# Performance work log

Measured on AMD Instinct MI355X. Metric: run time of the kernel, lower is better.

Reference implementation:

```python
import jax, jax.numpy as jnp
import numpy as np


def _slice_coeffs(grid, guide):
    """Trilinear slice of bilateral grid at (x, y, guide) per full-res pixel.
    grid:  [B, C, D, Hg, Wg]  (C=12 affine coeffs)
    guide: [B, 1, H, W] in [0, 1]
    returns coeffs [B, C, H, W]
    """
    B, C, D, Hg, Wg = grid.shape
    H, W = guide.shape[2], guide.shape[3]
    g = guide[:, 0]  # [B, H, W]

    # HDRNet sampling convention: pixel centers mapped into grid coords
    gx = (jnp.arange(W, dtype=grid.dtype) + 0.5) / W * Wg - 0.5   # [W]
    gy = (jnp.arange(H, dtype=grid.dtype) + 0.5) / H * Hg - 0.5   # [H]
    gz = g * D - 0.5                                              # [B, H, W]

    gx = jnp.broadcast_to(gx[None, None, :], (B, H, W))
    gy = jnp.broadcast_to(gy[None, :, None], (B, H, W))

    fx0 = jnp.floor(gx); fy0 = jnp.floor(gy); fz0 = jnp.floor(gz)
    wx = gx - fx0; wy = gy - fy0; wz = gz - fz0  # trilinear fractions

    x0 = jnp.clip(fx0.astype(jnp.int32), 0, Wg - 1)
    x1 = jnp.clip(fx0.astype(jnp.int32) + 1, 0, Wg - 1)
    y0 = jnp.clip(fy0.astype(jnp.int32), 0, Hg - 1)
    y1 = jnp.clip(fy0.astype(jnp.int32) + 1, 0, Hg - 1)
    z0 = jnp.clip(fz0.astype(jnp.int32), 0, D - 1)
    z1 = jnp.clip(fz0.astype(jnp.int32) + 1, 0, D - 1)

    def gather_one(gb, zi, yi, xi):
        # gb: [C, D, Hg, Wg]; zi/yi/xi: [H, W] -> [C, H, W]
        return gb[:, zi, yi, xi]

    gather = jax.vmap(gather_one)  # over batch

    out = jnp.zeros((B, C, H, W), dtype=grid.dtype)
    for zi, wzc in ((z0, 1.0 - wz), (z1, wz)):
        for yi, wyc in ((y0, 1.0 - wy), (y1, wy)):
            for xi, wxc in ((x0, 1.0 - wx), (x1, wx)):
                w = (wzc * wyc * wxc)[:, None]  # [B, 1, H, W]
                out = out + w * gather(grid, zi, yi, xi)
    return out


def setup_inputs() -> dict:
    key = jax.random.key(0)
    k1, k2, k3 = jax.random.split(key, 3)
    Bilterial_Grid = jax.random.normal(k1, (4, 12, 8, 16, 16), dtype=jnp.float32)
    Guide = jax.random.uniform(k2, (4, 1, 1024, 1024), dtype=jnp.float32)
    fr = jax.random.uniform(k3, (4, 3, 1024, 1024), dtype=jnp.float32)
    return {"Bilterial_Grid": Bilterial_Grid, "Guide": Guide, "fr": fr}


def reference(Bilterial_Grid, Guide, fr):
    B, _, H, W = fr.shape
    coeffs = _slice_coeffs(Bilterial_Grid, Guide)          # [B, 12, H, W]
    co = coeffs.reshape(B, 3, 4, H, W)                      # 3x4 affine per pixel
    # out_c = sum_i A[c,i] * fr_i + b[c]
    out = jnp.einsum('boihw,bihw->bohw', co[:, :, :3], fr) + co[:, :, 3]
    return out
```

## Files before the change

### kernel.cpp

```cpp
#include <hip/hip_runtime.h>


#define ZSTRIDE 132

static __device__ __forceinline__ unsigned short f2bf(float f) {
    unsigned int u = __float_as_uint(f);
    u += ((u >> 16) & 1u) + 0x7FFFu;
    return (unsigned short)(u >> 16);
}
static __device__ __forceinline__ float bf_lo(unsigned int d) {
    return __uint_as_float(d << 16);
}
static __device__ __forceinline__ float bf_hi(unsigned int d) {
    return __uint_as_float(d & 0xFFFF0000u);
}

static __device__ __forceinline__ void corner_fma(
    const unsigned int* __restrict__ cp, float wl, float wh,
    float& a0, float& a1, float& a2, float& a3)
{
    const uint4 d = *reinterpret_cast<const uint4*>(cp);
    a0 = fmaf(wl, bf_lo(d.x), a0); a0 = fmaf(wh, bf_hi(d.x), a0);
    a1 = fmaf(wl, bf_lo(d.y), a1); a1 = fmaf(wh, bf_hi(d.y), a1);
    a2 = fmaf(wl, bf_lo(d.z), a2); a2 = fmaf(wh, bf_hi(d.z), a2);
    a3 = fmaf(wl, bf_lo(d.w), a3); a3 = fmaf(wh, bf_hi(d.w), a3);
}

__global__ __launch_bounds__(256, 3) void slice_apply(
    const float* __restrict__ grid,
    const float* __restrict__ guide,
    const float* __restrict__ fr,
    float* __restrict__ out)
{
    __shared__ __align__(16) unsigned int lds[8 * ZSTRIDE];

    const int b     = blockIdx.y;
    const int tileX = blockIdx.x & 15;
    const int tileY = blockIdx.x >> 4;
    const int t     = threadIdx.x;

    {
        const int py0 = min(max(tileY - 1, 0), 15);
        const int py1 = tileY;
        const int py2 = min(tileY + 1, 15);
        const int px0 = min(max(tileX - 1, 0), 15);
        const int px1 = tileX;
        const int px2 = min(tileX + 1, 15);
        for (int e = t; e < 8 * 9 * 12; e += 256) {
            const int c    = e % 12;
            const int cell = (e / 12) % 9;
            const int s    = e / 108;
            const int s2   = min(s + 1, 7);
            const int gy3  = cell / 3;
            const int gx3  = cell % 3;
            const int ry = (gy3 == 0) ? py0 : ((gy3 == 1) ? py1 : py2);
            const int rx = (gx3 == 0) ? px0 : ((gx3 == 1) ? px1 : px2);
            const int cb = (b * 12 + c) * 8;
            const int sp = ry * 16 + rx;
            const float lo = grid[(cb + s)  * 256 + sp];
            const float hi = grid[(cb + s2) * 256 + sp];
            lds[s * ZSTRIDE + cell * 12 + c] =
                (unsigned int)f2bf(lo) | ((unsigned int)f2bf(hi) << 16);
        }
    }
    __syncthreads();

    const int w   = t >> 6;
    const int l   = t & 63;
    const int by  = w >> 1;
    const int bx  = w & 1;
    const int lxq = l & 31;
    const int sub = l >> 5;

    const int xg = tileX * 64 + bx * 32 + lxq;
    const float wx = ((float)(bx * 32 + lxq) + 0.5f) * 0.015625f +
                     (0.5f - (float)bx);
    const float u1 = wx, u0 = 1.0f - wx;

    const int cof0 = ((by + 0) * 3 + (bx + 0)) * 12;
    const int cof1 = ((by + 0) * 3 + (bx + 1)) * 12;
    const int cof2 = ((by + 1) * 3 + (bx + 0)) * 12;
    const int cof3 = ((by + 1) * 3 + (bx + 1)) * 12;

    const int ybase = tileY * 64 + by * 32;

    for (int i = 0; i < 16; ++i) {
        const int ly = by * 32 + i * 2 + sub;
        const int y  = ybase - by * 32 + ly;
        const float wy = ((float)ly + 0.5f) * 0.015625f + (0.5f - (float)by);
        const float v1 = wy, v0 = 1.0f - wy;

        const int gofs = (b * 1024 + y) * 1024 + xg;
        const int fofs = ((b * 3) * 1024 + y) * 1024 + xg;

        const float g  = guide[gofs];
        const float f0 = fr[fofs];
        const float f1 = fr[fofs + 1048576];
        const float f2 = fr[fofs + 2097152];

        const float gz = g * 8.0f - 0.5f;
        int s = (int)floorf(gz);
        s = min(max(s, 0), 7);
        const float wz = fmaxf(gz - (float)s, 0.0f);
        const float zl = 1.0f - wz, zh = wz;
        const unsigned int* sb = &lds[s * ZSTRIDE];

        const float w00 = v0 * u0, w01 = v0 * u1;
        const float w10 = v1 * u0, w11 = v1 * u1;
        const float wl0 = w00 * zl, wh0 = w00 * zh;
        const float wl1 = w01 * zl, wh1 = w01 * zh;
        const float wl2 = w10 * zl, wh2 = w10 * zh;
        const float wl3 = w11 * zl, wh3 = w11 * zh;

        float o0, o1, o2;
        {
            float a0 = 0.f, a1 = 0.f, a2 = 0.f, a3 = 0.f;
            corner_fma(sb + cof0, wl0, wh0, a0, a1, a2, a3);
            corner_fma(sb + cof1, wl1, wh1, a0, a1, a2, a3);
            corner_fma(sb + cof2, wl2, wh2, a0, a1, a2, a3);
            corner_fma(sb + cof3, wl3, wh3, a0, a1, a2, a3);
            o0 = fmaf(a0, f0, fmaf(a1, f1, fmaf(a2, f2, a3)));
        }
        {
            float a0 = 0.f, a1 = 0.f, a2 = 0.f, a3 = 0.f;
            corner_fma(sb + cof0 + 4, wl0, wh0, a0, a1, a2, a3);
            corner_fma(sb + cof1 + 4, wl1, wh1, a0, a1, a2, a3);
            corner_fma(sb + cof2 + 4, wl2, wh2, a0, a1, a2, a3);
            corner_fma(sb + cof3 + 4, wl3, wh3, a0, a1, a2, a3);
            o1 = fmaf(a0, f0, fmaf(a1, f1, fmaf(a2, f2, a3)));
        }
        {
            float a0 = 0.f, a1 = 0.f, a2 = 0.f, a3 = 0.f;
            corner_fma(sb + cof0 + 8, wl0, wh0, a0, a1, a2, a3);
            corner_fma(sb + cof1 + 8, wl1, wh1, a0, a1, a2, a3);
            corner_fma(sb + cof2 + 8, wl2, wh2, a0, a1, a2, a3);
            corner_fma(sb + cof3 + 8, wl3, wh3, a0, a1, a2, a3);
            o2 = fmaf(a0, f0, fmaf(a1, f1, fmaf(a2, f2, a3)));
        }

        out[fofs]           = o0;
        out[fofs + 1048576] = o1;
        out[fofs + 2097152] = o2;
    }
}

extern "C" void kernel_launch(void* const* d_in, const int* in_sizes, int n_in,
                              void* d_out, int out_size, void* d_ws, size_t ws_size,
                              hipStream_t stream) {
    const float* grid  = (const float*)d_in[0];
    const float* guide = (const float*)d_in[1];
    const float* fr    = (const float*)d_in[2];
    float* out = (float*)d_out;

    dim3 g(256, 4);
    dim3 blk(256);
    hipLaunchKernelGGL(slice_apply, g, blk, 0, stream, grid, guide, fr, out);
}
```

Measured before the change: 123.3 us.

## Process two pixels per thread with float2 accesses and register prefetch

Each thread now handles two adjacent pixels per row, using float2 loads and stores for guide, fr and out. Global loads for the next row are issued before the current row is computed, giving a software-pipelined double buffer in registers. The aim is fewer memory instructions and more loads in flight to hide latency. The cost is higher register pressure, which may reduce occupancy under the launch bounds, and a redundant reload on the last iteration.

Measured after the change: 126.6 us. 2.7% more time.

```diff
diff --git a/kernel.cpp b/kernel.cpp
--- a/kernel.cpp
+++ b/kernel.cpp
@@ -24,6 +24,53 @@
     a1 = fmaf(wl, bf_lo(d.y), a1); a1 = fmaf(wh, bf_hi(d.y), a1);
     a2 = fmaf(wl, bf_lo(d.z), a2); a2 = fmaf(wh, bf_hi(d.z), a2);
     a3 = fmaf(wl, bf_lo(d.w), a3); a3 = fmaf(wh, bf_hi(d.w), a3);
+}
+
+static __device__ __forceinline__ void pixel_compute(
+    const unsigned int* __restrict__ lds,
+    int cof0, int cof1, int cof2, int cof3,
+    float g, float u0, float u1, float v0, float v1,
+    float f0, float f1, float f2,
+    float& o0, float& o1, float& o2)
+{
+    const float gz = g * 8.0f - 0.5f;
+    int s = (int)floorf(gz);
+    s = min(max(s, 0), 7);
+    const float wz = fmaxf(gz - (float)s, 0.0f);
+    const float zl = 1.0f - wz, zh = wz;
+    const unsigned int* sb = lds + s * ZSTRIDE;
+
+    const float w00 = v0 * u0, w01 = v0 * u1;
+    const float w10 = v1 * u0, w11 = v1 * u1;
+    const float wl0 = w00 * zl, wh0 = w00 * zh;
+    const float wl1 = w01 * zl, wh1 = w01 * zh;
+    const float wl2 = w10 * zl, wh2 = w10 * zh;
+    const float wl3 = w11 * zl, wh3 = w11 * zh;
+
+    {
+        float a0 = 0.f, a1 = 0.f, a2 = 0.f, a3 = 0.f;
+        corner_fma(sb + cof0, wl0, wh0, a0, a1, a2, a3);
+        corner_fma(sb + cof1, wl1, wh1, a0, a1, a2, a3);
+        corner_fma(sb + cof2, wl2, wh2, a0, a1, a2, a3);
+        corner_fma(sb + cof3, wl3, wh3, a0, a1, a2, a3);
+        o0 = fmaf(a0, f0, fmaf(a1, f1, fmaf(a2, f2, a3)));
+    }
+    {
+        float a0 = 0.f, a1 = 0.f, a2 = 0.f, a3 = 0.f;
+        corner_fma(sb + cof0 + 4, wl0, wh0, a0, a1, a2, a3);
+        corner_fma(sb + cof1 + 4, wl1, wh1, a0, a1, a2, a3);
+        corner_fma(sb + cof2 + 4, wl2, wh2, a0, a1, a2, a3);
+        corner_fma(sb + cof3 + 4, wl3, wh3, a0, a1, a2, a3);
+        o1 = fmaf(a0, f0, fmaf(a1, f1, fmaf(a2, f2, a3)));
+    }
+    {
+        float a0 = 0.f, a1 = 0.f, a2 = 0.f, a3 = 0.f;
+        corner_fma(sb + cof0 + 8, wl0, wh0, a0, a1, a2, a3);
+        corner_fma(sb + cof1 + 8, wl1, wh1, a0, a1, a2, a3);
+        corner_fma(sb + cof2 + 8, wl2, wh2, a0, a1, a2, a3);
+        corner_fma(sb + cof3 + 8, wl3, wh3, a0, a1, a2, a3);
+        o2 = fmaf(a0, f0, fmaf(a1, f1, fmaf(a2, f2, a3)));
+    }
 }
 
 __global__ __launch_bounds__(256, 3) void slice_apply(
@@ -65,83 +112,89 @@
     }
     __syncthreads();
 
-    const int w   = t >> 6;
-    const int l   = t & 63;
-    const int by  = w >> 1;
-    const int bx  = w & 1;
-    const int lxq = l & 31;
-    const int sub = l >> 5;
-
-    const int xg = tileX * 64 + bx * 32 + lxq;
-    const float wx = ((float)(bx * 32 + lxq) + 0.5f) * 0.015625f +
-                     (0.5f - (float)bx);
-    const float u1 = wx, u0 = 1.0f - wx;
+    const int w    = t >> 6;
+    const int l    = t & 63;
+    const int by   = w >> 1;
+    const int bx   = w & 1;
+    const int row  = l >> 4;
+    const int xi   = (l & 15) * 2;
+    const int xloc = bx * 32 + xi;
+    const int xg   = tileX * 64 + xloc;
+
+    const float wxa = ((float)xloc + 0.5f) * 0.015625f + (0.5f - (float)bx);
+    const float wxb = ((float)xloc + 1.5f) * 0.015625f + (0.5f - (float)bx);
+    const float u00 = 1.0f - wxa, u01 = wxa;
+    const float u10 = 1.0f - wxb, u11 = wxb;
 
     const int cof0 = ((by + 0) * 3 + (bx + 0)) * 12;
     const int cof1 = ((by + 0) * 3 + (bx + 1)) * 12;
     const int cof2 = ((by + 1) * 3 + (bx + 0)) * 12;
     const int cof3 = ((by + 1) * 3 + (bx + 1)) * 12;
 
-    const int ybase = tileY * 64 + by * 32;
-
-    for (int i = 0; i < 16; ++i) {
-        const int ly = by * 32 + i * 2 + sub;
-        const int y  = ybase - by * 32 + ly;
-        const float wy = ((float)ly + 0.5f) * 0.015625f + (0.5f - (float)by);
-        const float v1 = wy, v0 = 1.0f - wy;
-
-        const int gofs = (b * 1024 + y) * 1024 + xg;
-        const int fofs = ((b * 3) * 1024 + y) * 1024 + xg;
-
-        const float g  = guide[gofs];
-        const float f0 = fr[fofs];
-        const float f1 = fr[fofs + 1048576];
-        const float f2 = fr[fofs + 2097152];
-
-        const float gz = g * 8.0f - 0.5f;
-        int s = (int)floorf(gz);
-        s = min(max(s, 0), 7);
-        const float wz = fmaxf(gz - (float)s, 0.0f);
-        const float zl = 1.0f - wz, zh = wz;
-        const unsigned int* sb = &lds[s * ZSTRIDE];
-
-        const float w00 = v0 * u0, w01 = v0 * u1;
-        const float w10 = v1 * u0, w11 = v1 * u1;
-        const float wl0 = w00 * zl, wh0 = w00 * zh;
-        const float wl1 = w01 * zl, wh1 = w01 * zh;
-        const float wl2 = w10 * zl, wh2 = w10 * zh;
-        const float wl3 = w11 * zl, wh3 = w11 * zh;
-
-        float o0, o1, o2;
-        {
-            float a0 = 0.f, a1 = 0.f, a2 = 0.f, a3 = 0.f;
-            corner_fma(sb + cof0, wl0, wh0, a0, a1, a2, a3);
-            corner_fma(sb + cof1, wl1, wh1, a0, a1, a2, a3);
-            corner_fma(sb + cof2, wl2, wh2, a0, a1, a2, a3);
-            corner_fma(sb + cof3, wl3, wh3, a0, a1, a2, a3);
-            o0 = fmaf(a0, f0, fmaf(a1, f1, fmaf(a2, f2, a3)));
-        }
-        {
-            float a0 = 0.f, a1 = 0.f, a2 = 0.f, a3 = 0.f;
-            corner_fma(sb + cof0 + 4, wl0, wh0, a0, a1, a2, a3);
-            corner_fma(sb + cof1 + 4, wl1, wh1, a0, a1, a2, a3);
-            corner_fma(sb + cof2 + 4, wl2, wh2, a0, a1, a2, a3);
-            corner_fma(sb + cof3 + 4, wl3, wh3, a0, a1, a2, a3);
-            o1 = fmaf(a0, f0, fmaf(a1, f1, fmaf(a2, f2, a3)));
-        }
-        {
-            float a0 = 0.f, a1 = 0.f, a2 = 0.f, a3 = 0.f;
-            corner_fma(sb + cof0 + 8, wl0, wh0, a0, a1, a2, a3);
-            corner_fma(sb + cof1 + 8, wl1, wh1, a0, a1, a2, a3);
-            corner_fma(sb + cof2 + 8, wl2, wh2, a0, a1, a2, a3);
-            corner_fma(sb + cof3 + 8, wl3, wh3, a0, a1, a2, a3);
-            o2 = fmaf(a0, f0, fmaf(a1, f1, fmaf(a2, f2, a3)));
-        }
-
-        out[fofs]           = o0;
-        out[fofs + 1048576] = o1;
-        out[fofs + 2097152] = o2;
-    }
+    const int lyb = by * 32 + row;
+    const int yb  = tileY * 64 + lyb;
+
+    #define GOFS(i) ((b * 1024 + yb + (i) * 4) * 1024 + xg)
+    #define FOFS(i) (((b * 3) * 1024 + yb + (i) * 4) * 1024 + xg)
+
+    float2 gc, c0, c1, c2, gn, n0, n1, n2;
+    {
+        const int go = GOFS(0), fo = FOFS(0);
+        gc = *reinterpret_cast<const float2*>(guide + go);
+        c0 = *reinterpret_cast<const float2*>(fr + fo);
+        c1 = *reinterpret_cast<const float2*>(fr + fo + 1048576);
+        c2 = *reinterpret_cast<const float2*>(fr + fo + 2097152);
+    }
+
+    for (int i = 0; i < 8; i += 2) {
+        {
+            const int go = GOFS(i + 1), fo = FOFS(i + 1);
+            gn = *reinterpret_cast<const float2*>(guide + go);
+            n0 = *reinterpret_cast<const float2*>(fr + fo);
+            n1 = *reinterpret_cast<const float2*>(fr + fo + 1048576);
+            n2 = *reinterpret_cast<const float2*>(fr + fo + 2097152);
+        }
+        {
+            const int ly = lyb + i * 4;
+            const float wy = ((float)ly + 0.5f) * 0.015625f + (0.5f - (float)by);
+            const float v1 = wy, v0 = 1.0f - wy;
+            float oa0, oa1, oa2, ob0, ob1, ob2;
+            pixel_compute(lds, cof0, cof1, cof2, cof3, gc.x, u00, u01, v0, v1,
+                          c0.x, c1.x, c2.x, oa0, oa1, oa2);
+            pixel_compute(lds, cof0, cof1, cof2, cof3, gc.y, u10, u11, v0, v1,
+                          c0.y, c1.y, c2.y, ob0, ob1, ob2);
+            const int fo = FOFS(i);
+            const float2 O0 = {oa0, ob0}, O1 = {oa1, ob1}, O2 = {oa2, ob2};
+            *reinterpret_cast<float2*>(out + fo)           = O0;
+            *reinterpret_cast<float2*>(out + fo + 1048576) = O1;
+            *reinterpret_cast<float2*>(out + fo + 2097152) = O2;
+        }
+        {
+            const int j  = min(i + 2, 7);
+            const int go = GOFS(j), fo = FOFS(j);
+            gc = *reinterpret_cast<const float2*>(guide + go);
+            c0 = *reinterpret_cast<const float2*>(fr + fo);
+            c1 = *reinterpret_cast<const float2*>(fr + fo + 1048576);
+            c2 = *reinterpret_cast<const float2*>(fr + fo + 2097152);
+        }
+        {
+            const int ly = lyb + (i + 1) * 4;
+            const float wy = ((float)ly + 0.5f) * 0.015625f + (0.5f - (float)by);
+            const float v1 = wy, v0 = 1.0f - wy;
+            float oa0, oa1, oa2, ob0, ob1, ob2;
+            pixel_compute(lds, cof0, cof1, cof2, cof3, gn.x, u00, u01, v0, v1,
+                          n0.x, n1.x, n2.x, oa0, oa1, oa2);
+            pixel_compute(lds, cof0, cof1, cof2, cof3, gn.y, u10, u11, v0, v1,
+                          n0.y, n1.y, n2.y, ob0, ob1, ob2);
+            const int fo = FOFS(i + 1);
+            const float2 O0 = {oa0, ob0}, O1 = {oa1, ob1}, O2 = {oa2, ob2};
+            *reinterpret_cast<float2*>(out + fo)           = O0;
+            *reinterpret_cast<float2*>(out + fo + 1048576) = O1;
+            *reinterpret_cast<float2*>(out + fo + 2097152) = O2;
+        }
+    }
+    #undef GOFS
+    #undef FOFS
 }
 
 extern "C" void kernel_launch(void* const* d_in, const int* in_sizes, int n_in,
```
